# Performance work log

Measured on AMD Instinct MI355X. Metric: run time of the kernel, lower is better.

## Reference

```python
import jax, jax.numpy as jnp
import numpy as np

# bone-direction joint pairs (pred A-B vs target A-B), order: pelvis_bal, chest_bal,
# mid_spine, r_u_leg, l_u_leg, r_l_leg, l_l_leg, r_foot, l_foot, r_u_arm, l_u_arm,
# r_l_arm, l_l_arm
_PA = np.array([2, 14, 6, 5, 4, 8, 7, 11, 10, 19, 18, 21, 20])
_PB = np.array([1, 13, 3, 2, 1, 5, 4, 8, 7, 17, 16, 19, 18])
_TA = np.array([22, 11, 2, 23, 19, 24, 20, 25, 21, 13, 6, 14, 7])
_TB = np.array([18, 4, 1, 22, 18, 23, 19, 24, 20, 12, 5, 13, 6])


def _cos_mean(a, b):
    # a, b: [..., 3]; cosine over last axis, mean over all leading axes -> scalar (or [13])
    num = jnp.sum(a * b, axis=-1)
    den = jnp.linalg.norm(a, axis=-1) * jnp.linalg.norm(b, axis=-1)
    return jnp.mean(num / den, axis=0)


def setup_inputs() -> dict:
    key = jax.random.key(0)
    k1, k2, k3, k4 = jax.random.split(key, 4)
    B = 1_000_000
    return {
        "scale": jnp.ones((1,), jnp.float32),
        "smpl_index": jax.random.randint(k3, (14,), 0, 24, dtype=jnp.int32),
        "dataset_index": jax.random.randint(k4, (14,), 0, 26, dtype=jnp.int32),
        "pred_jtr": jax.random.normal(k1, (B, 24, 3), jnp.float32),
        "target_jtr": jax.random.normal(k2, (B, 26, 3), jnp.float32),
    }


def reference(scale, smpl_index, dataset_index, pred_jtr, target_jtr):
    # smooth L1 (beta = 1.0, mean reduction)
    d = scale[0] * pred_jtr[:, smpl_index, :] - target_jtr[:, dataset_index, :]
    ad = jnp.abs(d)
    jtr_loss = jnp.mean(jnp.where(ad < 1.0, 0.5 * d * d, ad - 0.5))

    # cross-product orientation terms (pelvis + chest)
    p_pelvis = jnp.cross(pred_jtr[:, 2] - pred_jtr[:, 0], pred_jtr[:, 1] - pred_jtr[:, 0])
    t_pelvis = jnp.cross(target_jtr[:, 22] - target_jtr[:, 1], target_jtr[:, 18] - target_jtr[:, 1])
    p_chest = jnp.cross(pred_jtr[:, 13] - pred_jtr[:, 9], pred_jtr[:, 14] - pred_jtr[:, 9])
    t_chest = jnp.cross(target_jtr[:, 3] - target_jtr[:, 2], target_jtr[:, 11] - target_jtr[:, 2])
    pelvis_ori = _cos_mean(p_pelvis, t_pelvis)
    chest_ori = _cos_mean(p_chest, t_chest)

    # 13 bone-direction cosine terms, fully vectorized: [B, 13, 3]
    vp = pred_jtr[:, _PA, :] - pred_jtr[:, _PB, :]
    vt = target_jtr[:, _TA, :] - target_jtr[:, _TB, :]
    dir_cos = _cos_mean(vp, vt)  # [13]

    loss = (jtr_loss + (1.0 - pelvis_ori) + (1.0 - chest_ori)
            + jnp.sum(1.0 - dir_cos))
    return (loss, jtr_loss)
```

## Files before the change

### kernel.cpp

```cpp
#include <hip/hip_runtime.h>

#define DEV __device__ __forceinline__

struct F3 { float x, y, z; };
DEV F3 mk3(float a, float b, float c) { F3 r; r.x = a; r.y = b; r.z = c; return r; }
DEV F3 sub3(F3 a, F3 b) { return mk3(a.x - b.x, a.y - b.y, a.z - b.z); }
DEV F3 cross3(F3 a, F3 b) {
    return mk3(a.y*b.z - a.z*b.y, a.z*b.x - a.x*b.z, a.x*b.y - a.y*b.x);
}
DEV float cosv(F3 a, F3 b) {
    float num = a.x*b.x + a.y*b.y + a.z*b.z;
    float na  = a.x*a.x + a.y*a.y + a.z*a.z;
    float nb  = b.x*b.x + b.y*b.y + b.z*b.z;
    return num * rsqrtf(na * nb);
}

constexpr int ROWS = 64;
constexpr int TPB  = 64;
constexpr int PSTR = 73;
constexpr int TSTR = 79;
constexpr int LDS_BYTES = ROWS * (PSTR + TSTR) * 4;
constexpr int NBMAX = 1024;

constexpr int TG4  = ROWS * 78 / 4;
constexpr int NT4  = 19;

__global__ __launch_bounds__(TPB, 1) void ori_loss_main(
    const float* __restrict__ scale,
    const int*   __restrict__ sidx,
    const int*   __restrict__ didx,
    const float* __restrict__ pred,
    const float* __restrict__ targ,
    int B, int ntiles, int nb,
    float* __restrict__ partial)
{
    extern __shared__ float lds[];
    float* lp = lds;
    float* lt = lds + ROWS * PSTR;

    const int tid = threadIdx.x;
    const float s = scale[0];

    int sj[14], dj[14];
    #pragma unroll
    for (int k = 0; k < 14; ++k) { sj[k] = sidx[k] * 3; dj[k] = didx[k] * 3; }

    const float4* gp = (const float4*)pred;
    const float4* gt4 = (const float4*)targ;
    const long maxp = (long)B * 18 - 1;
    const long maxt4 = (long)B * 78 / 4 - 1;

    float4 bp[18];
    float4 bt[NT4 + 1];

    auto load_pred = [&](int t) {
        long basep = (long)t * (ROWS * 18);
        #pragma unroll
        for (int k = 0; k < 18; ++k) {
            long i = basep + tid + TPB * k;
            bp[k] = gp[i > maxp ? maxp : i];
        }
    };
    auto load_targ = [&](int t) {
        long baset = (long)t * TG4;
        #pragma unroll
        for (int k = 0; k < NT4; ++k) {
            long i = baset + tid + TPB * k;
            bt[k] = gt4[i > maxt4 ? maxt4 : i];
        }
        {
            long i = baset + NT4 * TPB + tid;
            bt[NT4] = gt4[i > maxt4 ? maxt4 : i];
        }
    };

    auto put_targ = [&](int gg, float4 v) {
        int f = gg * 4;
        int r = f / 78;
        int j = f - r * 78;
        float* d = lt + r * TSTR + j;
        if (j < 76) {
            d[0] = v.x; d[1] = v.y; d[2] = v.z; d[3] = v.w;
        } else {
            d[0] = v.x; d[1] = v.y;
            float* d2 = lt + (r + 1) * TSTR;
            d2[0] = v.z; d2[1] = v.w;
        }
    };

    float sumj = 0.0f, sumc = 0.0f;
    int t = blockIdx.x;
    load_targ(t);
    load_pred(t);

    for (;;) {
        int tn = t + nb;
        bool more = tn < ntiles;

        #pragma unroll
        for (int k = 0; k < NT4; ++k) put_targ(tid + TPB * k, bt[k]);
        if (tid < 32)              put_targ(tid + TPB * NT4, bt[NT4]);
        if (more) load_targ(tn);
        asm volatile("" ::: "memory");

        #pragma unroll
        for (int k = 0; k < 18; ++k) {
            int i = tid + TPB * k;
            int r = i / 18, j = i - r * 18;
            float* d = lp + r * PSTR + j * 4;
            d[0] = bp[k].x; d[1] = bp[k].y; d[2] = bp[k].z; d[3] = bp[k].w;
        }
        if (more) load_pred(tn);
        asm volatile("" ::: "memory");

        int rows = min(ROWS, B - t * ROWS);
        if (tid < rows) {
            const float* pr = lp + tid * PSTR;
            const float* tr = lt + tid * TSTR;

            #pragma unroll
            for (int k = 0; k < 14; ++k) {
                #pragma unroll
                for (int c = 0; c < 3; ++c) {
                    float d  = s * pr[sj[k] + c] - tr[dj[k] + c];
                    float ad = fabsf(d);
                    sumj += (ad < 1.0f) ? 0.5f * d * d : (ad - 0.5f);
                }
            }

            #define P3(j) mk3(pr[(j)*3], pr[(j)*3+1], pr[(j)*3+2])
            #define T3(j) mk3(tr[(j)*3], tr[(j)*3+1], tr[(j)*3+2])
            sumc += cosv(cross3(sub3(P3(2), P3(0)), sub3(P3(1), P3(0))),
                         cross3(sub3(T3(22), T3(1)), sub3(T3(18), T3(1))));
            sumc += cosv(cross3(sub3(P3(13), P3(9)), sub3(P3(14), P3(9))),
                         cross3(sub3(T3(3), T3(2)), sub3(T3(11), T3(2))));
            #define DIR(pa, pb, ta, tb) sumc += cosv(sub3(P3(pa), P3(pb)), sub3(T3(ta), T3(tb)));
            DIR(2, 1, 22, 18)
            DIR(14, 13, 11, 4)
            DIR(6, 3, 2, 1)
            DIR(5, 2, 23, 22)
            DIR(4, 1, 19, 18)
            DIR(8, 5, 24, 23)
            DIR(7, 4, 20, 19)
            DIR(11, 8, 25, 24)
            DIR(10, 7, 21, 20)
            DIR(19, 17, 13, 12)
            DIR(18, 16, 6, 5)
            DIR(21, 19, 14, 13)
            DIR(20, 18, 7, 6)
            #undef DIR
            #undef P3
            #undef T3
        }

        if (!more) break;
        t = tn;
    }

    #pragma unroll
    for (int off = 32; off; off >>= 1) {
        sumj += __shfl_down(sumj, off);
        sumc += __shfl_down(sumc, off);
    }
    if (tid == 0) {
        partial[blockIdx.x]      = sumj;
        partial[nb + blockIdx.x] = sumc;
    }
}

__global__ __launch_bounds__(256) void ori_loss_final(
    const float* __restrict__ partial, int nblk, int B, float* __restrict__ out)
{
    double dj = 0.0, dc = 0.0;
    for (int i = threadIdx.x; i < nblk; i += 256) {
        dj += (double)partial[i];
        dc += (double)partial[nblk + i];
    }
    #pragma unroll
    for (int off = 32; off; off >>= 1) {
        dj += __shfl_down(dj, off);
        dc += __shfl_down(dc, off);
    }
    __shared__ double wj[4], wc[4];
    int wid  = threadIdx.x >> 6;
    int lane = threadIdx.x & 63;
    if (lane == 0) { wj[wid] = dj; wc[wid] = dc; }
    __syncthreads();
    if (threadIdx.x == 0) {
        double J = wj[0] + wj[1] + wj[2] + wj[3];
        double C = wc[0] + wc[1] + wc[2] + wc[3];
        double jtr  = J / ((double)B * 42.0);
        double loss = jtr + 15.0 - C / (double)B;
        out[0] = (float)loss;
        out[1] = (float)jtr;
    }
}

extern "C" void kernel_launch(void* const* d_in, const int* in_sizes, int n_in,
                              void* d_out, int out_size, void* d_ws, size_t ws_size,
                              hipStream_t stream) {
    const float* scale = (const float*)d_in[0];
    const int*   sidx  = (const int*)d_in[1];
    const int*   didx  = (const int*)d_in[2];
    const float* pred  = (const float*)d_in[3];
    const float* targ  = (const float*)d_in[4];

    int B      = in_sizes[3] / 72;
    int ntiles = (B + ROWS - 1) / ROWS;
    int nb     = ntiles < NBMAX ? ntiles : NBMAX;

    float* partial = (float*)d_ws;
    float* out     = (float*)d_out;

    ori_loss_main<<<nb, TPB, LDS_BYTES, stream>>>(scale, sidx, didx, pred, targ,
                                                  B, ntiles, nb, partial);
    ori_loss_final<<<1, 256, 0, stream>>>(partial, nb, B, out);
}
```

Measured before the change: 113.3 us.

## Double-buffer register prefetch with smaller tiles and more resident blocks

```diff
diff --git a/kernel.cpp b/kernel.cpp
--- a/kernel.cpp
+++ b/kernel.cpp
@@ -15,17 +15,18 @@
     return num * rsqrtf(na * nb);
 }
 
-constexpr int ROWS = 64;
+constexpr int ROWS = 32;
 constexpr int TPB  = 64;
 constexpr int PSTR = 73;
 constexpr int TSTR = 79;
 constexpr int LDS_BYTES = ROWS * (PSTR + TSTR) * 4;
-constexpr int NBMAX = 1024;
-
+constexpr int NBMAX = 2048;
+
+constexpr int NP4  = ROWS * 18 / 64;
 constexpr int TG4  = ROWS * 78 / 4;
-constexpr int NT4  = 19;
-
-__global__ __launch_bounds__(TPB, 1) void ori_loss_main(
+constexpr int NT4F = 9;
+
+__global__ __launch_bounds__(TPB, 2) void ori_loss_main(
     const float* __restrict__ scale,
     const int*   __restrict__ sidx,
     const int*   __restrict__ didx,
@@ -45,34 +46,30 @@
     #pragma unroll
     for (int k = 0; k < 14; ++k) { sj[k] = sidx[k] * 3; dj[k] = didx[k] * 3; }
 
-    const float4* gp = (const float4*)pred;
+    const float4* gp  = (const float4*)pred;
     const float4* gt4 = (const float4*)targ;
-    const long maxp = (long)B * 18 - 1;
+    const long maxp  = (long)B * 18 - 1;
     const long maxt4 = (long)B * 78 / 4 - 1;
 
-    float4 bp[18];
-    float4 bt[NT4 + 1];
-
-    auto load_pred = [&](int t) {
-        long basep = (long)t * (ROWS * 18);
-        #pragma unroll
-        for (int k = 0; k < 18; ++k) {
-            long i = basep + tid + TPB * k;
-            bp[k] = gp[i > maxp ? maxp : i];
-        }
-    };
-    auto load_targ = [&](int t) {
-        long baset = (long)t * TG4;
-        #pragma unroll
-        for (int k = 0; k < NT4; ++k) {
-            long i = baset + tid + TPB * k;
-            bt[k] = gt4[i > maxt4 ? maxt4 : i];
-        }
-        {
-            long i = baset + NT4 * TPB + tid;
-            bt[NT4] = gt4[i > maxt4 ? maxt4 : i];
-        }
-    };
+    float4 bpA[NP4], btA[NT4F + 1];
+    float4 bpB[NP4], btB[NT4F + 1];
+
+#define LOAD_PRED(buf, t)                                                      \
+    { long basep = (long)(t) * (ROWS * 18);                                    \
+      _Pragma("unroll")                                                        \
+      for (int k = 0; k < NP4; ++k) {                                          \
+          long i = basep + tid + TPB * k;                                      \
+          buf[k] = gp[i > maxp ? maxp : i];                                    \
+      } }
+#define LOAD_TARG(buf, t)                                                      \
+    { long baset = (long)(t) * TG4;                                            \
+      _Pragma("unroll")                                                        \
+      for (int k = 0; k < NT4F; ++k) {                                         \
+          long i = baset + tid + TPB * k;                                      \
+          buf[k] = gt4[i > maxt4 ? maxt4 : i];                                 \
+      }                                                                        \
+      { long i = baset + NT4F * TPB + tid;    \
+        buf[NT4F] = gt4[i > maxt4 ? maxt4 : i]; } }
 
     auto put_targ = [&](int gg, float4 v) {
         int f = gg * 4;
@@ -87,32 +84,22 @@
             d2[0] = v.z; d2[1] = v.w;
         }
     };
+    auto put_pred = [&](int gg, float4 v) {
+        int r = gg / 18, j = gg - r * 18;
+        float* d = lp + r * PSTR + j * 4;
+        d[0] = v.x; d[1] = v.y; d[2] = v.z; d[3] = v.w;
+    };
+
+#define WRITE_TILE(bt, bp)                                                     \
+    { _Pragma("unroll")                                                        \
+      for (int k = 0; k < NT4F; ++k) put_targ(tid + TPB * k, bt[k]);           \
+      if (tid < TG4 - NT4F * TPB) put_targ(tid + TPB * NT4F, bt[NT4F]);        \
+      _Pragma("unroll")                                                        \
+      for (int k = 0; k < NP4; ++k) put_pred(tid + TPB * k, bp[k]); }
 
     float sumj = 0.0f, sumc = 0.0f;
-    int t = blockIdx.x;
-    load_targ(t);
-    load_pred(t);
-
-    for (;;) {
-        int tn = t + nb;
-        bool more = tn < ntiles;
-
-        #pragma unroll
-        for (int k = 0; k < NT4; ++k) put_targ(tid + TPB * k, bt[k]);
-        if (tid < 32)              put_targ(tid + TPB * NT4, bt[NT4]);
-        if (more) load_targ(tn);
-        asm volatile("" ::: "memory");
-
-        #pragma unroll
-        for (int k = 0; k < 18; ++k) {
-            int i = tid + TPB * k;
-            int r = i / 18, j = i - r * 18;
-            float* d = lp + r * PSTR + j * 4;
-            d[0] = bp[k].x; d[1] = bp[k].y; d[2] = bp[k].z; d[3] = bp[k].w;
-        }
-        if (more) load_pred(tn);
-        asm volatile("" ::: "memory");
-
+
+    auto compute = [&](int t) {
         int rows = min(ROWS, B - t * ROWS);
         if (tid < rows) {
             const float* pr = lp + tid * PSTR;
@@ -152,9 +139,34 @@
             #undef P3
             #undef T3
         }
-
-        if (!more) break;
-        t = tn;
+    };
+
+    int t = blockIdx.x;
+    LOAD_TARG(btA, t)
+    LOAD_PRED(bpA, t)
+    {
+        int t1 = t + nb;
+        if (t1 < ntiles) { LOAD_TARG(btB, t1) LOAD_PRED(bpB, t1) }
+    }
+
+    for (;;) {
+        int t1 = t + nb, t2 = t + 2 * nb;
+
+        WRITE_TILE(btA, bpA)
+        if (t2 < ntiles) { LOAD_TARG(btA, t2) LOAD_PRED(bpA, t2) }
+        asm volatile("" ::: "memory");
+        compute(t);
+        if (t1 >= ntiles) break;
+
+        {
+            int t3 = t + 3 * nb;
+            WRITE_TILE(btB, bpB)
+            if (t3 < ntiles) { LOAD_TARG(btB, t3) LOAD_PRED(bpB, t3) }
+        }
+        asm volatile("" ::: "memory");
+        compute(t1);
+        if (t2 >= ntiles) break;
+        t = t2;
     }
 
     #pragma unroll
@@ -166,6 +178,9 @@
         partial[blockIdx.x]      = sumj;
         partial[nb + blockIdx.x] = sumc;
     }
+#undef LOAD_PRED
+#undef LOAD_TARG
+#undef WRITE_TILE
 }
 
 __global__ __launch_bounds__(256) void ori_loss_final(
```

Measured after the change: 249.8 us. 121% more time.
